# Performance work log

Hardware: AMD Instinct MI355X
Metric: run time of the kernel (lower is better)

The kernel has to match this reference:

```python
import jax
import jax.numpy as jnp
import numpy as np

NPOINT = 512
RADIUS = 0.2
K = 32


def setup_inputs() -> dict:
    key = jax.random.key(0)
    k1, k2 = jax.random.split(key)
    xyz = jax.random.uniform(k1, (8, 16384, 3), dtype=jnp.float32)      # [B,N,3] in unit cube
    features = jax.random.normal(k2, (8, 128, 16384), dtype=jnp.float32)  # [B,D,N]
    return {"xyz": xyz, "features": features}


def farthest_point_sample(xyz, npoint):
    # xyz: [B,N,3] -> centroids [B,npoint] int32. Deterministic start at index 0
    # (the torch code does randint(...)*0).
    B, N, _ = xyz.shape
    init_dist = jnp.full((B, N), 1e10, dtype=xyz.dtype)
    init_far = jnp.zeros((B,), dtype=jnp.int32)

    def step(carry, _):
        distance, farthest = carry
        centroid = jnp.take_along_axis(xyz, farthest[:, None, None], axis=1)  # [B,1,3]
        d = jnp.sum((xyz - centroid) ** 2, axis=-1)                           # [B,N]
        distance = jnp.minimum(distance, d)
        new_far = jnp.argmax(distance, axis=-1).astype(jnp.int32)
        return (distance, new_far), farthest

    (_, _), cents = jax.lax.scan(step, (init_dist, init_far), None, length=npoint)
    return cents.T  # [B, npoint]


def square_distance(src, dst):
    # src [B,S,3], dst [B,N,3] -> [B,S,N]
    d = -2.0 * jnp.einsum("bsc,bnc->bsn", src, dst)
    d = d + jnp.sum(src ** 2, -1)[:, :, None]
    d = d + jnp.sum(dst ** 2, -1)[:, None, :]
    return d


def query_ball_point(radius, nsample, xyz, new_xyz):
    B, N, _ = xyz.shape
    sqrd = square_distance(new_xyz, xyz)                              # [B,S,N]
    arangeN = jnp.arange(N, dtype=jnp.int32)[None, None, :]
    idx = jnp.where(sqrd > radius ** 2, N, arangeN)                   # out-of-ball -> sentinel N
    idx = jnp.sort(idx, axis=-1)[:, :, :nsample]                      # [B,S,K]
    first = idx[:, :, :1]
    idx = jnp.where(idx == N, first, idx)                             # pad with first valid neighbor
    return idx


def index_points(points, idx):
    # points [B,N,C], idx [B,...] -> [B,...,C]
    B = points.shape[0]
    bidx = jnp.arange(B).reshape((B,) + (1,) * (idx.ndim - 1))
    return points[bidx, idx]


def reference(xyz, features):
    # xyz [B,N,3], features [B,D,N]
    cent = farthest_point_sample(xyz, NPOINT)                 # [B,S]
    new_xyz = index_points(xyz, cent)                         # [B,S,3]
    idx = query_ball_point(RADIUS, K, xyz, new_xyz)           # [B,S,K]
    pts = jnp.transpose(features, (0, 2, 1))                  # [B,N,D]
    grouped = index_points(pts, idx)                          # [B,S,K,D]
    sub_features = jnp.max(grouped, axis=2)                   # [B,S,D]  (max over K neighbors)
    sub_features = jnp.transpose(sub_features, (0, 2, 1))     # [B,D,S]
    return new_xyz, sub_features
```

## Files before the change

### kernel.cpp

```cpp
#include <hip/hip_runtime.h>
#include <stdint.h>
#include <math.h>

#define NB      8
#define NPTS    16384
#define NPOINT  512
#define NCH     128
#define KNBR    32
#define R2      0.04f

#define DPP_ARG_STEP(v, p, CTRL) do {                                          \
    float _ov = __builtin_bit_cast(float, __builtin_amdgcn_update_dpp(         \
        __builtin_bit_cast(int, (v)), __builtin_bit_cast(int, (v)),            \
        (CTRL), 0xF, 0xF, false));                                             \
    int _op = __builtin_amdgcn_update_dpp((p), (p), (CTRL), 0xF, 0xF, false);  \
    bool _t = (_ov > (v)) || ((_ov == (v)) && (_op < (p)));                    \
    (v) = _t ? _ov : (v);                                                      \
    (p) = _t ? _op : (p);                                                      \
} while (0)

#define SHFL_ARG_STEP(v, p, XORAMT) do {                                       \
    float _ov = __shfl_xor((v), (XORAMT), 64);                                 \
    int   _op = __shfl_xor((p), (XORAMT), 64);                                 \
    bool _t = (_ov > (v)) || ((_ov == (v)) && (_op < (p)));                    \
    (v) = _t ? _ov : (v);                                                      \
    (p) = _t ? _op : (p);                                                      \
} while (0)

__global__
__attribute__((amdgpu_flat_work_group_size(1024, 1024)))
__attribute__((amdgpu_waves_per_eu(4, 4)))
__attribute__((amdgpu_num_vgpr(128)))
void fps_transpose_kernel(const float* __restrict__ xyz,
                          const float* __restrict__ feat,
                          float* __restrict__ out,
                          int* __restrict__ cent,
                          float* __restrict__ ft,
                          int use_ft)
{
    const int blk = blockIdx.x;
    const int tid = threadIdx.x;

    if (blk < NB) {
        const int b = blk;
        const float* xb = xyz + (size_t)b * NPTS * 3;
        float px[16], py[16], pz[16], dist[16];
#pragma unroll
        for (int k = 0; k < 16; ++k) {
            int p = k * 1024 + tid;
            px[k] = xb[p * 3 + 0];
            py[k] = xb[p * 3 + 1];
            pz[k] = xb[p * 3 + 2];
            dist[k] = 1e10f;
        }
        __shared__ float s_v[2][16];
        __shared__ int   s_p[2][16];
        const int lane = tid & 63;
        const int wid  = tid >> 6;

        float cx = xb[0], cy = xb[1], cz = xb[2];
        if (tid == 0) {
            cent[b * NPOINT + 0] = 0;
            out[((size_t)b * NPOINT + 0) * 3 + 0] = cx;
            out[((size_t)b * NPOINT + 0) * 3 + 1] = cy;
            out[((size_t)b * NPOINT + 0) * 3 + 2] = cz;
        }

        for (int i = 1; i < NPOINT; ++i) {
            float bv = -1.0f; int bk = 0;
#pragma unroll
            for (int k = 0; k < 16; ++k) {
                float dx = __fsub_rn(px[k], cx);
                float dy = __fsub_rn(py[k], cy);
                float dz = __fsub_rn(pz[k], cz);
                float d  = __fadd_rn(__fadd_rn(__fmul_rn(dx, dx),
                                               __fmul_rn(dy, dy)),
                                     __fmul_rn(dz, dz));
                float nd = fminf(dist[k], d);
                dist[k] = nd;
                if (nd > bv) { bv = nd; bk = k; }
            }
            float rv = bv;
            int   rp = bk * 1024 + tid;
            DPP_ARG_STEP(rv, rp, 0xB1);
            DPP_ARG_STEP(rv, rp, 0x4E);
            DPP_ARG_STEP(rv, rp, 0x141);
            DPP_ARG_STEP(rv, rp, 0x140);
            SHFL_ARG_STEP(rv, rp, 16);
            SHFL_ARG_STEP(rv, rp, 32);
            const int buf = i & 1;
            if (lane == 0) { s_v[buf][wid] = rv; s_p[buf][wid] = rp; }
            __syncthreads();
            float fv = s_v[buf][lane & 15];
            int   fp = s_p[buf][lane & 15];
            DPP_ARG_STEP(fv, fp, 0xB1);
            DPP_ARG_STEP(fv, fp, 0x4E);
            DPP_ARG_STEP(fv, fp, 0x141);
            DPP_ARG_STEP(fv, fp, 0x140);
            const int cur = __builtin_amdgcn_readfirstlane(fp);
            cx = xb[cur * 3 + 0];
            cy = xb[cur * 3 + 1];
            cz = xb[cur * 3 + 2];
            if (tid == 0) {
                cent[b * NPOINT + i] = cur;
                size_t o = ((size_t)b * NPOINT + i) * 3;
                out[o + 0] = cx; out[o + 1] = cy; out[o + 2] = cz;
            }
        }
    } else {
        if (!use_ft) return;
        int t  = blk - NB;
        int b  = t >> 11;
        int r  = t & 2047;
        int ct = r >> 9;
        int nt = r & 511;
        __shared__ float tile[32][33];
        int tx = tid & 31, ty = tid >> 5;
        int c = ct * 32 + ty, n = nt * 32 + tx;
        tile[ty][tx] = feat[((size_t)b * NCH + c) * NPTS + n];
        __syncthreads();
        int n2 = nt * 32 + ty, c2 = ct * 32 + tx;
        ft[((size_t)b * NPTS + n2) * NCH + c2] = tile[tx][ty];
    }
}

__global__ __launch_bounds__(256, 4)
void query_pool_kernel(const float* __restrict__ xyz,
                       const float* __restrict__ feat,
                       const float* __restrict__ ft,
                       const int* __restrict__ cent,
                       float* __restrict__ out_sub,
                       int use_ft)
{
    const int tid  = threadIdx.x;
    const int widx = tid >> 6;
    const int lane = tid & 63;
    const int w = blockIdx.x * 4 + widx;
    const int b = w >> 9;
    const int s = w & 511;

    const float* xb = xyz + (size_t)b * NPTS * 3;
    const int ci = cent[b * NPOINT + s];
    const float sx = xb[ci * 3 + 0];
    const float sy = xb[ci * 3 + 1];
    const float sz = xb[ci * 3 + 2];
    const float snorm = __fadd_rn(__fadd_rn(__fmul_rn(sx, sx),
                                            __fmul_rn(sy, sy)),
                                  __fmul_rn(sz, sz));

    __shared__ int lidx[4][KNBR];
    int found = 0;
    for (int base = 0; base < NPTS && found < KNBR; base += 64) {
        int j = base + lane;
        float dx = xb[j * 3 + 0];
        float dy = xb[j * 3 + 1];
        float dz = xb[j * 3 + 2];
        float dn = __fadd_rn(__fadd_rn(__fmul_rn(dx, dx),
                                       __fmul_rn(dy, dy)),
                             __fmul_rn(dz, dz));
        float dot = __fadd_rn(__fadd_rn(__fmul_rn(sx, dx),
                                        __fmul_rn(sy, dy)),
                              __fmul_rn(sz, dz));
        float d = __fadd_rn(__fadd_rn(__fmul_rn(-2.0f, dot), snorm), dn);
        bool inball = !(d > R2);
        unsigned long long mask = __ballot(inball);
        int before = (int)__popcll(mask & ((1ULL << lane) - 1ULL));
        int slot = found + before;
        if (inball && slot < KNBR) lidx[widx][slot] = j;
        found += (int)__popcll(mask);
    }
    int cnt = found < KNBR ? found : KNBR;
    __syncthreads();

    float a0 = -INFINITY, a1 = -INFINITY;
    if (use_ft) {
        for (int m = 0; m < cnt; ++m) {
            int i = lidx[widx][m];
            const float* row = ft + ((size_t)b * NPTS + i) * NCH;
            a0 = fmaxf(a0, row[lane]);
            a1 = fmaxf(a1, row[lane + 64]);
        }
    } else {
        for (int m = 0; m < cnt; ++m) {
            int i = lidx[widx][m];
            a0 = fmaxf(a0, feat[((size_t)b * NCH + lane) * NPTS + i]);
            a1 = fmaxf(a1, feat[((size_t)b * NCH + lane + 64) * NPTS + i]);
        }
    }
    out_sub[((size_t)b * NCH + lane) * NPOINT + s] = a0;
    out_sub[((size_t)b * NCH + lane + 64) * NPOINT + s] = a1;
}

extern "C" void kernel_launch(void* const* d_in, const int* in_sizes, int n_in,
                              void* d_out, int out_size, void* d_ws, size_t ws_size,
                              hipStream_t stream)
{
    const float* xyz  = (const float*)d_in[0];
    const float* feat = (const float*)d_in[1];
    float* out = (float*)d_out;

    int*   cent = (int*)d_ws;
    float* ft   = (float*)((char*)d_ws + 16384);
    const size_t need_ft = 16384ull + (size_t)NB * NPTS * NCH * 4ull;
    int use_ft = (ws_size >= need_ft) ? 1 : 0;

    int nblocks1 = use_ft ? (NB + NB * (NCH / 32) * (NPTS / 32)) : NB;
    hipLaunchKernelGGL(fps_transpose_kernel, dim3(nblocks1), dim3(1024), 0, stream,
                       xyz, feat, out, cent, ft, use_ft);

    hipLaunchKernelGGL(query_pool_kernel, dim3((NB * NPOINT) / 4), dim3(256), 0, stream,
                       xyz, feat, ft, cent, out + (size_t)NB * NPOINT * 3, use_ft);
}
```

Measured before the change: 1.175 ms.

## Split FPS per batch across 8 cooperating blocks with global-memory slot exchange

Farthest point sampling for each batch now runs on 8 blocks of 256 threads instead of one 1024-thread block. Each block handles 2048 points and publishes its per-iteration argmax as a packed 64-bit value tagged with the iteration. All 8 blocks spin on relaxed agent-scope atomics until every slot carries the current iteration, then reduce the 8 candidates with shuffles. The aim is to spread the serial FPS loop over more CUs, at the cost of a cross-block barrier every iteration that depends on all 64 blocks being co-resident, with a guard counter as a fallback. The transpose blocks now use 256 threads, each moving four elements.

```diff
diff --git a/kernel.cpp b/kernel.cpp
--- a/kernel.cpp
+++ b/kernel.cpp
@@ -8,6 +8,13 @@
 #define NCH     128
 #define KNBR    32
 #define R2      0.04f
+
+#define FPSB    8
+#define FPSPTS  (NPTS / FPSB)
+#define FPST    256
+#define FPSK    (FPSPTS / FPST)
+
+typedef unsigned long long u64;
 
 #define DPP_ARG_STEP(v, p, CTRL) do {                                          \
     float _ov = __builtin_bit_cast(float, __builtin_amdgcn_update_dpp(         \
@@ -27,39 +34,50 @@
     (p) = _t ? _op : (p);                                                      \
 } while (0)
 
-__global__
-__attribute__((amdgpu_flat_work_group_size(1024, 1024)))
-__attribute__((amdgpu_waves_per_eu(4, 4)))
-__attribute__((amdgpu_num_vgpr(128)))
+#define SHFL_ARG_STEP_U(v, p, XORAMT) do {                                     \
+    unsigned _ov = __shfl_xor((v), (XORAMT), 64);                              \
+    unsigned _op = __shfl_xor((p), (XORAMT), 64);                              \
+    bool _t = (_ov > (v)) || ((_ov == (v)) && (_op < (p)));                    \
+    (v) = _t ? _ov : (v);                                                      \
+    (p) = _t ? _op : (p);                                                      \
+} while (0)
+
+__global__ __launch_bounds__(FPST, 2)
 void fps_transpose_kernel(const float* __restrict__ xyz,
                           const float* __restrict__ feat,
                           float* __restrict__ out,
                           int* __restrict__ cent,
+                          u64* __restrict__ slots,
                           float* __restrict__ ft,
                           int use_ft)
 {
     const int blk = blockIdx.x;
     const int tid = threadIdx.x;
 
-    if (blk < NB) {
-        const int b = blk;
+    if (blk < NB * FPSB) {
+        const int b = blk >> 3;
+        const int j = blk & 7;
+        const int base = j * FPSPTS;
         const float* xb = xyz + (size_t)b * NPTS * 3;
-        float px[16], py[16], pz[16], dist[16];
-#pragma unroll
-        for (int k = 0; k < 16; ++k) {
-            int p = k * 1024 + tid;
+        u64* bs0 = slots + 0 * NB * FPSB + b * FPSB;
+        u64* bs1 = slots + 1 * NB * FPSB + b * FPSB;
+
+        float px[FPSK], py[FPSK], pz[FPSK], dist[FPSK];
+#pragma unroll
+        for (int k = 0; k < FPSK; ++k) {
+            int p = base + k * FPST + tid;
             px[k] = xb[p * 3 + 0];
             py[k] = xb[p * 3 + 1];
             pz[k] = xb[p * 3 + 2];
             dist[k] = 1e10f;
         }
-        __shared__ float s_v[2][16];
-        __shared__ int   s_p[2][16];
+        __shared__ float s_v[2][4];
+        __shared__ int   s_p[2][4];
         const int lane = tid & 63;
         const int wid  = tid >> 6;
 
         float cx = xb[0], cy = xb[1], cz = xb[2];
-        if (tid == 0) {
+        if (j == 0 && tid == 0) {
             cent[b * NPOINT + 0] = 0;
             out[((size_t)b * NPOINT + 0) * 3 + 0] = cx;
             out[((size_t)b * NPOINT + 0) * 3 + 1] = cy;
@@ -69,7 +87,7 @@
         for (int i = 1; i < NPOINT; ++i) {
             float bv = -1.0f; int bk = 0;
 #pragma unroll
-            for (int k = 0; k < 16; ++k) {
+            for (int k = 0; k < FPSK; ++k) {
                 float dx = __fsub_rn(px[k], cx);
                 float dy = __fsub_rn(py[k], cy);
                 float dz = __fsub_rn(pz[k], cz);
@@ -81,7 +99,7 @@
                 if (nd > bv) { bv = nd; bk = k; }
             }
             float rv = bv;
-            int   rp = bk * 1024 + tid;
+            int   rp = base + bk * FPST + tid;
             DPP_ARG_STEP(rv, rp, 0xB1);
             DPP_ARG_STEP(rv, rp, 0x4E);
             DPP_ARG_STEP(rv, rp, 0x141);
@@ -89,19 +107,39 @@
             SHFL_ARG_STEP(rv, rp, 16);
             SHFL_ARG_STEP(rv, rp, 32);
             const int buf = i & 1;
+            u64* bslots = buf ? bs1 : bs0;
             if (lane == 0) { s_v[buf][wid] = rv; s_p[buf][wid] = rp; }
             __syncthreads();
-            float fv = s_v[buf][lane & 15];
-            int   fp = s_p[buf][lane & 15];
+            float fv = s_v[buf][lane & 3];
+            int   fp = s_p[buf][lane & 3];
             DPP_ARG_STEP(fv, fp, 0xB1);
             DPP_ARG_STEP(fv, fp, 0x4E);
-            DPP_ARG_STEP(fv, fp, 0x141);
-            DPP_ARG_STEP(fv, fp, 0x140);
-            const int cur = __builtin_amdgcn_readfirstlane(fp);
+            if (tid == 0) {
+                u64 pk = ((u64)__builtin_bit_cast(unsigned, fv) << 32)
+                       | (u64)(((unsigned)i << 14) | (unsigned)fp);
+                __hip_atomic_store(&bslots[j], pk, __ATOMIC_RELAXED,
+                                   __HIP_MEMORY_SCOPE_AGENT);
+            }
+            const int jj = lane & 7;
+            u64 got = 0;
+            int guard = 0;
+            for (;;) {
+                got = __hip_atomic_load(&bslots[jj], __ATOMIC_RELAXED,
+                                        __HIP_MEMORY_SCOPE_AGENT);
+                bool ok = (((unsigned)got) >> 14) == (unsigned)i;
+                if (__ballot(ok) == ~0ull) break;
+                if (++guard > (1 << 20)) break;
+            }
+            unsigned wv = (unsigned)(got >> 32);
+            unsigned wp = (unsigned)got & 0x3FFFu;
+            SHFL_ARG_STEP_U(wv, wp, 1);
+            SHFL_ARG_STEP_U(wv, wp, 2);
+            SHFL_ARG_STEP_U(wv, wp, 4);
+            const int cur = (int)__builtin_amdgcn_readfirstlane(wp);
             cx = xb[cur * 3 + 0];
             cy = xb[cur * 3 + 1];
             cz = xb[cur * 3 + 2];
-            if (tid == 0) {
+            if (j == 0 && tid == 0) {
                 cent[b * NPOINT + i] = cur;
                 size_t o = ((size_t)b * NPOINT + i) * 3;
                 out[o + 0] = cx; out[o + 1] = cy; out[o + 2] = cz;
@@ -109,18 +147,26 @@
         }
     } else {
         if (!use_ft) return;
-        int t  = blk - NB;
+        int t  = blk - NB * FPSB;
         int b  = t >> 11;
         int r  = t & 2047;
         int ct = r >> 9;
         int nt = r & 511;
         __shared__ float tile[32][33];
         int tx = tid & 31, ty = tid >> 5;
-        int c = ct * 32 + ty, n = nt * 32 + tx;
-        tile[ty][tx] = feat[((size_t)b * NCH + c) * NPTS + n];
+        int n = nt * 32 + tx;
+#pragma unroll
+        for (int rr = 0; rr < 4; ++rr) {
+            int c = ct * 32 + ty + rr * 8;
+            tile[ty + rr * 8][tx] = feat[((size_t)b * NCH + c) * NPTS + n];
+        }
         __syncthreads();
-        int n2 = nt * 32 + ty, c2 = ct * 32 + tx;
-        ft[((size_t)b * NPTS + n2) * NCH + c2] = tile[tx][ty];
+        int c2 = ct * 32 + tx;
+#pragma unroll
+        for (int rr = 0; rr < 4; ++rr) {
+            int n2 = nt * 32 + ty + rr * 8;
+            ft[((size_t)b * NPTS + n2) * NCH + c2] = tile[tx][ty + rr * 8];
+        }
     }
 }
 
@@ -199,14 +245,15 @@
     const float* feat = (const float*)d_in[1];
     float* out = (float*)d_out;
 
-    int*   cent = (int*)d_ws;
-    float* ft   = (float*)((char*)d_ws + 16384);
-    const size_t need_ft = 16384ull + (size_t)NB * NPTS * NCH * 4ull;
+    int*   cent  = (int*)d_ws;
+    u64*   slots = (u64*)((char*)d_ws + 16384);
+    float* ft    = (float*)((char*)d_ws + 32768);
+    const size_t need_ft = 32768ull + (size_t)NB * NPTS * NCH * 4ull;
     int use_ft = (ws_size >= need_ft) ? 1 : 0;
 
-    int nblocks1 = use_ft ? (NB + NB * (NCH / 32) * (NPTS / 32)) : NB;
-    hipLaunchKernelGGL(fps_transpose_kernel, dim3(nblocks1), dim3(1024), 0, stream,
-                       xyz, feat, out, cent, ft, use_ft);
+    int nblocks1 = NB * FPSB + (use_ft ? NB * (NCH / 32) * (NPTS / 32) : 0);
+    hipLaunchKernelGGL(fps_transpose_kernel, dim3(nblocks1), dim3(FPST), 0, stream,
+                       xyz, feat, out, cent, slots, ft, use_ft);
 
     hipLaunchKernelGGL(query_pool_kernel, dim3((NB * NPOINT) / 4), dim3(256), 0, stream,
                        xyz, feat, ft, cent, out + (size_t)NB * NPOINT * 3, use_ft);
```

Measured after the change: 1.356 ms. 1.15x slower.

## Morton-sort points and skip FPS distance updates per wave via bounding-box bounds

Applied to the files above, without the earlier changes.

Adds a pre-pass kernel that buckets each batch's points by a 9-bit Morton code, so each FPS wave owns a spatially compact group of points with a known bounding box. On each FPS iteration a wave computes a lower bound on the distance from the new centroid to its box. If that bound exceeds the wave's current best min-distance, it skips the 16-point distance update and the intra-wave argmax reduction, since none of its distances can change. Tie-breaking now compares original point indices so results match the reference order. The cost is an extra kernel launch, extra workspace, and scattered global writes in the sort, and the VGPR cap was removed.

```diff
diff --git a/kernel.cpp b/kernel.cpp
--- a/kernel.cpp
+++ b/kernel.cpp
@@ -8,6 +8,8 @@
 #define NCH     128
 #define KNBR    32
 #define R2      0.04f
+
+typedef unsigned long long u64;
 
 #define DPP_ARG_STEP(v, p, CTRL) do {                                          \
     float _ov = __builtin_bit_cast(float, __builtin_amdgcn_update_dpp(         \
@@ -27,11 +29,75 @@
     (p) = _t ? _op : (p);                                                      \
 } while (0)
 
+__global__ __launch_bounds__(1024, 4)
+void sort_kernel(const float* __restrict__ xyz,
+                 float* __restrict__ sx, float* __restrict__ sy,
+                 float* __restrict__ sz, int* __restrict__ sidx)
+{
+    const int b = blockIdx.x;
+    const int tid = threadIdx.x;
+    const float* xb = xyz + (size_t)b * NPTS * 3;
+    __shared__ int offs[512];
+    if (tid < 512) offs[tid] = 0;
+    __syncthreads();
+#pragma unroll
+    for (int k = 0; k < 16; ++k) {
+        int p = k * 1024 + tid;
+        float x = xb[p * 3 + 0], y = xb[p * 3 + 1], z = xb[p * 3 + 2];
+        int ix = (int)(x * 8.f); ix = ix < 0 ? 0 : (ix > 7 ? 7 : ix);
+        int iy = (int)(y * 8.f); iy = iy < 0 ? 0 : (iy > 7 ? 7 : iy);
+        int iz = (int)(z * 8.f); iz = iz < 0 ? 0 : (iz > 7 ? 7 : iz);
+        int m = 0;
+#pragma unroll
+        for (int j = 0; j < 3; ++j)
+            m |= ((ix >> j & 1) << (3 * j + 2)) | ((iy >> j & 1) << (3 * j + 1))
+               | ((iz >> j & 1) << (3 * j));
+        atomicAdd(&offs[m], 1);
+    }
+    __syncthreads();
+    if (tid < 64) {
+        int base = tid * 8, run = 0, v[8];
+#pragma unroll
+        for (int j = 0; j < 8; ++j) { v[j] = run; run += offs[base + j]; }
+        int own = run;
+        for (int off = 1; off < 64; off <<= 1) {
+            int t = __shfl_up(run, off, 64);
+            if (tid >= off) run += t;
+        }
+        int lane_excl = run - own;
+#pragma unroll
+        for (int j = 0; j < 8; ++j) offs[base + j] = lane_excl + v[j];
+    }
+    __syncthreads();
+    float* sxb = sx + (size_t)b * NPTS;
+    float* syb = sy + (size_t)b * NPTS;
+    float* szb = sz + (size_t)b * NPTS;
+    int*   sib = sidx + (size_t)b * NPTS;
+#pragma unroll
+    for (int k = 0; k < 16; ++k) {
+        int p = k * 1024 + tid;
+        float x = xb[p * 3 + 0], y = xb[p * 3 + 1], z = xb[p * 3 + 2];
+        int ix = (int)(x * 8.f); ix = ix < 0 ? 0 : (ix > 7 ? 7 : ix);
+        int iy = (int)(y * 8.f); iy = iy < 0 ? 0 : (iy > 7 ? 7 : iy);
+        int iz = (int)(z * 8.f); iz = iz < 0 ? 0 : (iz > 7 ? 7 : iz);
+        int m = 0;
+#pragma unroll
+        for (int j = 0; j < 3; ++j)
+            m |= ((ix >> j & 1) << (3 * j + 2)) | ((iy >> j & 1) << (3 * j + 1))
+               | ((iz >> j & 1) << (3 * j));
+        int pos = atomicAdd(&offs[m], 1);
+        sxb[pos] = x; syb[pos] = y; szb[pos] = z; sib[pos] = p;
+    }
+}
+
 __global__
 __attribute__((amdgpu_flat_work_group_size(1024, 1024)))
 __attribute__((amdgpu_waves_per_eu(4, 4)))
-__attribute__((amdgpu_num_vgpr(128)))
 void fps_transpose_kernel(const float* __restrict__ xyz,
+                          const float* __restrict__ sx,
+                          const float* __restrict__ sy,
+                          const float* __restrict__ sz,
+                          const int* __restrict__ sidx,
                           const float* __restrict__ feat,
                           float* __restrict__ out,
                           int* __restrict__ cent,
@@ -44,20 +110,43 @@
     if (blk < NB) {
         const int b = blk;
         const float* xb = xyz + (size_t)b * NPTS * 3;
+        const size_t sb = (size_t)b * NPTS;
+        const int lane = tid & 63;
+        const int wid  = tid >> 6;
+
         float px[16], py[16], pz[16], dist[16];
+        int   pid[16];
 #pragma unroll
         for (int k = 0; k < 16; ++k) {
-            int p = k * 1024 + tid;
-            px[k] = xb[p * 3 + 0];
-            py[k] = xb[p * 3 + 1];
-            pz[k] = xb[p * 3 + 2];
+            int p = wid * 1024 + k * 64 + lane;
+            px[k] = sx[sb + p];
+            py[k] = sy[sb + p];
+            pz[k] = sz[sb + p];
+            pid[k] = sidx[sb + p];
             dist[k] = 1e10f;
         }
+        float lox = px[0], hix = px[0], loy = py[0], hiy = py[0];
+        float loz = pz[0], hiz = pz[0];
+#pragma unroll
+        for (int k = 1; k < 16; ++k) {
+            lox = fminf(lox, px[k]); hix = fmaxf(hix, px[k]);
+            loy = fminf(loy, py[k]); hiy = fmaxf(hiy, py[k]);
+            loz = fminf(loz, pz[k]); hiz = fmaxf(hiz, pz[k]);
+        }
+        for (int off = 1; off < 64; off <<= 1) {
+            lox = fminf(lox, __shfl_xor(lox, off, 64));
+            hix = fmaxf(hix, __shfl_xor(hix, off, 64));
+            loy = fminf(loy, __shfl_xor(loy, off, 64));
+            hiy = fmaxf(hiy, __shfl_xor(hiy, off, 64));
+            loz = fminf(loz, __shfl_xor(loz, off, 64));
+            hiz = fmaxf(hiz, __shfl_xor(hiz, off, 64));
+        }
+
         __shared__ float s_v[2][16];
         __shared__ int   s_p[2][16];
-        const int lane = tid & 63;
-        const int wid  = tid >> 6;
-
+
+        float cbv = 1e10f;
+        int   cbp = 0x7FFFFFFF;
         float cx = xb[0], cy = xb[1], cz = xb[2];
         if (tid == 0) {
             cent[b * NPOINT + 0] = 0;
@@ -67,29 +156,36 @@
         }
 
         for (int i = 1; i < NPOINT; ++i) {
-            float bv = -1.0f; int bk = 0;
-#pragma unroll
-            for (int k = 0; k < 16; ++k) {
-                float dx = __fsub_rn(px[k], cx);
-                float dy = __fsub_rn(py[k], cy);
-                float dz = __fsub_rn(pz[k], cz);
-                float d  = __fadd_rn(__fadd_rn(__fmul_rn(dx, dx),
-                                               __fmul_rn(dy, dy)),
-                                     __fmul_rn(dz, dz));
-                float nd = fminf(dist[k], d);
-                dist[k] = nd;
-                if (nd > bv) { bv = nd; bk = k; }
+            float gx = fmaxf(fmaxf(__fsub_rn(lox, cx), __fsub_rn(cx, hix)), 0.f);
+            float gy = fmaxf(fmaxf(__fsub_rn(loy, cy), __fsub_rn(cy, hiy)), 0.f);
+            float gz = fmaxf(fmaxf(__fsub_rn(loz, cz), __fsub_rn(cz, hiz)), 0.f);
+            float lb = gx * gx + gy * gy + gz * gz;
+            if (!(lb * 0.999995f >= cbv)) {
+                float bv = -1.0f; int bp = 0x7FFFFFFF;
+#pragma unroll
+                for (int k = 0; k < 16; ++k) {
+                    float dx = __fsub_rn(px[k], cx);
+                    float dy = __fsub_rn(py[k], cy);
+                    float dz = __fsub_rn(pz[k], cz);
+                    float d  = __fadd_rn(__fadd_rn(__fmul_rn(dx, dx),
+                                                   __fmul_rn(dy, dy)),
+                                         __fmul_rn(dz, dz));
+                    float nd = fminf(dist[k], d);
+                    dist[k] = nd;
+                    bool t = (nd > bv) || ((nd == bv) && (pid[k] < bp));
+                    bv = t ? nd : bv;
+                    bp = t ? pid[k] : bp;
+                }
+                DPP_ARG_STEP(bv, bp, 0xB1);
+                DPP_ARG_STEP(bv, bp, 0x4E);
+                DPP_ARG_STEP(bv, bp, 0x141);
+                DPP_ARG_STEP(bv, bp, 0x140);
+                SHFL_ARG_STEP(bv, bp, 16);
+                SHFL_ARG_STEP(bv, bp, 32);
+                cbv = bv; cbp = bp;
             }
-            float rv = bv;
-            int   rp = bk * 1024 + tid;
-            DPP_ARG_STEP(rv, rp, 0xB1);
-            DPP_ARG_STEP(rv, rp, 0x4E);
-            DPP_ARG_STEP(rv, rp, 0x141);
-            DPP_ARG_STEP(rv, rp, 0x140);
-            SHFL_ARG_STEP(rv, rp, 16);
-            SHFL_ARG_STEP(rv, rp, 32);
             const int buf = i & 1;
-            if (lane == 0) { s_v[buf][wid] = rv; s_p[buf][wid] = rp; }
+            if (lane == 0) { s_v[buf][wid] = cbv; s_p[buf][wid] = cbp; }
             __syncthreads();
             float fv = s_v[buf][lane & 15];
             int   fp = s_p[buf][lane & 15];
@@ -141,12 +237,12 @@
 
     const float* xb = xyz + (size_t)b * NPTS * 3;
     const int ci = cent[b * NPOINT + s];
-    const float sx = xb[ci * 3 + 0];
-    const float sy = xb[ci * 3 + 1];
-    const float sz = xb[ci * 3 + 2];
-    const float snorm = __fadd_rn(__fadd_rn(__fmul_rn(sx, sx),
-                                            __fmul_rn(sy, sy)),
-                                  __fmul_rn(sz, sz));
+    const float sxc = xb[ci * 3 + 0];
+    const float syc = xb[ci * 3 + 1];
+    const float szc = xb[ci * 3 + 2];
+    const float snorm = __fadd_rn(__fadd_rn(__fmul_rn(sxc, sxc),
+                                            __fmul_rn(syc, syc)),
+                                  __fmul_rn(szc, szc));
 
     __shared__ int lidx[4][KNBR];
     int found = 0;
@@ -158,9 +254,9 @@
         float dn = __fadd_rn(__fadd_rn(__fmul_rn(dx, dx),
                                        __fmul_rn(dy, dy)),
                              __fmul_rn(dz, dz));
-        float dot = __fadd_rn(__fadd_rn(__fmul_rn(sx, dx),
-                                        __fmul_rn(sy, dy)),
-                              __fmul_rn(sz, dz));
+        float dot = __fadd_rn(__fadd_rn(__fmul_rn(sxc, dx),
+                                        __fmul_rn(syc, dy)),
+                              __fmul_rn(szc, dz));
         float d = __fadd_rn(__fadd_rn(__fmul_rn(-2.0f, dot), snorm), dn);
         bool inball = !(d > R2);
         unsigned long long mask = __ballot(inball);
@@ -199,14 +295,23 @@
     const float* feat = (const float*)d_in[1];
     float* out = (float*)d_out;
 
-    int*   cent = (int*)d_ws;
-    float* ft   = (float*)((char*)d_ws + 16384);
-    const size_t need_ft = 16384ull + (size_t)NB * NPTS * NCH * 4ull;
+    const size_t NBP = (size_t)NB * NPTS;
+    char* w = (char*)d_ws;
+    int*   cent = (int*)w;                        w += 16384;
+    float* sx   = (float*)w;                      w += NBP * 4;
+    float* sy   = (float*)w;                      w += NBP * 4;
+    float* sz   = (float*)w;                      w += NBP * 4;
+    int*   sidx = (int*)w;                        w += NBP * 4;
+    float* ft   = (float*)w;
+    const size_t need_ft = (size_t)(w - (char*)d_ws) + NBP * NCH * 4ull;
     int use_ft = (ws_size >= need_ft) ? 1 : 0;
 
-    int nblocks1 = use_ft ? (NB + NB * (NCH / 32) * (NPTS / 32)) : NB;
+    hipLaunchKernelGGL(sort_kernel, dim3(NB), dim3(1024), 0, stream,
+                       xyz, sx, sy, sz, sidx);
+
+    int nblocks1 = NB + (use_ft ? NB * (NCH / 32) * (NPTS / 32) : 0);
     hipLaunchKernelGGL(fps_transpose_kernel, dim3(nblocks1), dim3(1024), 0, stream,
-                       xyz, feat, out, cent, ft, use_ft);
+                       xyz, sx, sy, sz, sidx, feat, out, cent, ft, use_ft);
 
     hipLaunchKernelGGL(query_pool_kernel, dim3((NB * NPOINT) / 4), dim3(256), 0, stream,
                        xyz, feat, ft, cent, out + (size_t)NB * NPOINT * 3, use_ft);
```

Result: slower. 1.228 ms (+4.5%).
